# Kernel optimization log

Hardware: AMD Instinct MI355X
Metric: run time of the kernel (lower is better)

Reference implementation:

```python
import jax, jax.numpy as jnp
import numpy as np

DIM = 768
NUM_HEADS = 12
HEAD_DIM = DIM // NUM_HEADS
SCALE = HEAD_DIM ** -0.5
B, N = 16, 640  # N = 8*8 + 24*24


def setup_inputs() -> dict:
    key = jax.random.key(0)
    ks = jax.random.split(key, 4)
    x = jax.random.normal(ks[0], (B, N, DIM), dtype=jnp.float32)
    # weights stored input-major: y = x @ W + b (equiv. to torch Linear with W = weight.T)
    qkv_w = jax.random.normal(ks[1], (DIM, 3 * DIM), dtype=jnp.float32) * (DIM ** -0.5)
    qkv_b = jnp.zeros((3 * DIM,), dtype=jnp.float32)
    proj_w = jax.random.normal(ks[2], (DIM, DIM), dtype=jnp.float32) * (DIM ** -0.5)
    proj_b = jnp.zeros((DIM,), dtype=jnp.float32)
    w = jnp.ones((2,), dtype=jnp.float32)
    return {"x": x, "qkv_w": qkv_w, "qkv_b": qkv_b, "proj_w": proj_w,
            "proj_b": proj_b, "w": w, "t_h": 8, "t_w": 8, "s_h": 24, "s_w": 24}


def reference(x, qkv_w, qkv_b, proj_w, proj_b, w, t_h, t_w, s_h, s_w):
    b, n, c = x.shape
    qkv = (x @ qkv_w + qkv_b).reshape(b, n, 3, NUM_HEADS, HEAD_DIM)
    qkv = jnp.transpose(qkv, (2, 0, 3, 1, 4))  # [3, B, H, N, D]
    q, k, v = qkv[0], qkv[1], qkv[2]
    attn = jnp.einsum('bhnd,bhmd->bhnm', q, k) * SCALE  # [B,H,N,N]
    attn0 = jax.nn.softmax(attn, axis=-1)
    attn1 = jnp.square(jax.nn.relu(attn))
    ws = jax.nn.softmax(w)  # exp(w_i)/sum(exp(w)) blend weights
    attn = attn0 * ws[0] + attn1 * ws[1]
    out = jnp.einsum('bhnm,bhmd->bhnd', attn, v)  # [B,H,N,D]
    out = jnp.transpose(out, (0, 2, 1, 3)).reshape(b, n, c)
    return out @ proj_w + proj_b
```

## Files before the change

kernel.cpp:

```cpp
#include <hip/hip_runtime.h>
#include <hip/hip_bf16.h>

typedef __attribute__((ext_vector_type(8))) short short8;
typedef __attribute__((ext_vector_type(4))) float floatx4;
typedef __hip_bfloat16 bf16;

#define DIM 768
#define NH 12
#define HD 64
#define BB 16
#define NN 640
#define BH (BB*NH)
#define MROWS (BB*NN)
#define QKVN (3*DIM)
#define QSCALE 0.18033688011113205f
#define LN2SQ 0.4804530139182014f

#define CVT_BLK (MROWS*DIM/4/256)
#define TRQ_BLK ((QKVN/32)*(DIM/32))
#define TRP_BLK ((DIM/32)*(DIM/32))

__device__ __forceinline__ floatx4 mfma16(short8 a, short8 b, floatx4 c) {
    return __builtin_amdgcn_mfma_f32_16x16x32_bf16(a, b, c, 0, 0, 0);
}

__device__ __forceinline__ void async_ld16(const bf16* g, bf16* l) {
    __builtin_amdgcn_global_load_lds(
        (const __attribute__((address_space(1))) void*)g,
        (__attribute__((address_space(3))) void*)l, 16, 0, 0);
}

__device__ __forceinline__ unsigned pack_trunc(float a, float b) {
    return __builtin_amdgcn_perm(__float_as_uint(b), __float_as_uint(a), 0x07060302u);
}

__device__ __forceinline__ float fexp2(float x) {
#if __has_builtin(__builtin_amdgcn_exp2f)
    return __builtin_amdgcn_exp2f(x);
#else
    return exp2f(x);
#endif
}

__global__ void prep_all(const float* __restrict__ x,
                         const float* __restrict__ qkv_w,
                         const float* __restrict__ proj_w,
                         bf16* __restrict__ xb,
                         bf16* __restrict__ qwT,
                         bf16* __restrict__ pwT)
{
    __shared__ float tile[32][33];
    const int id = blockIdx.x;
    const int t = threadIdx.x;

    if (id < CVT_BLK) {
        int i = id * 256 + t;
        float4 v = ((const float4*)x)[i];
        bf16* p = xb + (size_t)i * 4;
        p[0] = __float2bfloat16(v.x);
        p[1] = __float2bfloat16(v.y);
        p[2] = __float2bfloat16(v.z);
        p[3] = __float2bfloat16(v.w);
        return;
    }

    const float* src; bf16* dst; int C, bx, by;
    if (id < CVT_BLK + TRQ_BLK) {
        int j = id - CVT_BLK;
        bx = j % (QKVN/32); by = j / (QKVN/32);
        src = qkv_w; dst = qwT; C = QKVN;
    } else {
        int j = id - CVT_BLK - TRQ_BLK;
        bx = j % (DIM/32); by = j / (DIM/32);
        src = proj_w; dst = pwT; C = DIM;
    }
    const int R = DIM;
    const int tx = t & 31, ty = t >> 5;
    for (int j = 0; j < 4; ++j)
        tile[ty + j*8][tx] = src[(size_t)(by*32 + ty + j*8) * C + bx*32 + tx];
    __syncthreads();
    for (int j = 0; j < 4; ++j)
        dst[(size_t)(bx*32 + ty + j*8) * R + by*32 + tx] = __float2bfloat16(tile[tx][ty + j*8]);
}

template<int MODE>
__global__ __launch_bounds__(256) void gemm_bt(
    const bf16* __restrict__ A, const bf16* __restrict__ B, const float* __restrict__ bias,
    int M, int N, int K,
    bf16* __restrict__ outb, bf16* __restrict__ vTo, float* __restrict__ outf)
{
    __shared__ __align__(16) bf16 As[2][128*64];
    __shared__ __align__(16) bf16 Bs[2][128*64];

    const int t = threadIdx.x;
    const int lane = t & 63, wave = t >> 6;
    const int l15 = lane & 15, quad = lane >> 4;
    const int wm = (wave >> 1) * 64, wn = (wave & 1) * 64;
    const int m0 = blockIdx.y * 128, n0 = blockIdx.x * 128;

    floatx4 acc[4][4];
    floatx4 zero = {0.f, 0.f, 0.f, 0.f};
    for (int i = 0; i < 4; ++i)
        for (int j = 0; j < 4; ++j)
            acc[i][j] = zero;

    const int trow = t >> 3;
    const int gc = ((t & 7) ^ (trow & 7)) << 3;
    const bf16* aA = A + (size_t)(m0 + trow) * K + gc;
    const bf16* aB = B + (size_t)(n0 + trow) * K + gc;
    const int lb = wave * 512;

    for (int s = 0; s < 4; ++s) {
        async_ld16(aA + (size_t)s*32*K, &As[0][s*2048 + lb]);
        async_ld16(aB + (size_t)s*32*K, &Bs[0][s*2048 + lb]);
    }

    const int sw = l15 & 7;
    const int nit = K >> 6;
    for (int kt = 0; kt < nit; ++kt) {
        const int cur = kt & 1;
        __syncthreads();
        if (kt + 1 < nit) {
            const bf16* pA = aA + (size_t)(kt+1)*64;
            const bf16* pB = aB + (size_t)(kt+1)*64;
            for (int s = 0; s < 4; ++s) {
                async_ld16(pA + (size_t)s*32*K, &As[cur^1][s*2048 + lb]);
                async_ld16(pB + (size_t)s*32*K, &Bs[cur^1][s*2048 + lb]);
            }
        }
        short8 af0[4], af1[4], bf0[4], bf1[4];
        for (int fm = 0; fm < 4; ++fm) {
            int base = (wm + fm*16 + l15) * 64 + ((quad ^ sw) << 3);
            af0[fm] = *(const short8*)(&As[cur][base]);
            af1[fm] = *(const short8*)(&As[cur][base ^ 32]);
        }
        for (int fn = 0; fn < 4; ++fn) {
            int base = (wn + fn*16 + l15) * 64 + ((quad ^ sw) << 3);
            bf0[fn] = *(const short8*)(&Bs[cur][base]);
            bf1[fn] = *(const short8*)(&Bs[cur][base ^ 32]);
        }
        for (int fm = 0; fm < 4; ++fm)
            for (int fn = 0; fn < 4; ++fn) {
                acc[fm][fn] = mfma16(af0[fm], bf0[fn], acc[fm][fn]);
                acc[fm][fn] = mfma16(af1[fm], bf1[fn], acc[fm][fn]);
            }
    }

    if (MODE == 0 && n0 >= 2*DIM) {
        bf16* T4 = &As[0][0] + wave * 2048;
        const int bh   = (m0 / NN) * NH + ((n0 + wn) >> 6) - 24;
        const int tokb = (m0 % NN) + wm;
        for (int fn = 0; fn < 4; ++fn) {
            int n = n0 + wn + fn*16 + l15;
            float bn = bias[n];
            for (int fm = 0; fm < 4; ++fm) {
                float v0 = acc[fm][fn][0] + bn, v1 = acc[fm][fn][1] + bn;
                float v2 = acc[fm][fn][2] + bn, v3 = acc[fm][fn][3] + bn;
                *(uint2*)(T4 + fm*512 + l15*32 + quad*4) =
                    make_uint2(pack_trunc(v0, v1), pack_trunc(v2, v3));
            }
            uint4 r0 = *(const uint4*)(T4 + quad*512 + l15*32);
            uint4 r1 = *(const uint4*)(T4 + quad*512 + l15*32 + 8);
            int d = fn*16 + l15;
            bf16* dst = vTo + ((size_t)bh * HD + d) * NN + tokb + quad*16;
            *(uint4*)dst = r0;
            *(uint4*)(dst + 8) = r1;
        }
        return;
    }

    for (int fm = 0; fm < 4; ++fm) {
        for (int fn = 0; fn < 4; ++fn) {
            int n = n0 + wn + fn*16 + l15;
            float bn = bias[n];
            for (int r = 0; r < 4; ++r) {
                int m = m0 + wm + fm*16 + quad*4 + r;
                float v = acc[fm][fn][r] + bn;
                if (MODE == 0) {
                    if (n < DIM) v *= QSCALE;
                    outb[(size_t)m * N + n] = __float2bfloat16(v);
                } else {
                    outf[(size_t)m * N + n] = v;
                }
            }
        }
    }
}

__global__ __launch_bounds__(256) void attn_kernel(
    const bf16* __restrict__ qkv, const bf16* __restrict__ vT,
    const float* __restrict__ w2, bf16* __restrict__ ao)
{
    const int bh = blockIdx.x;
    const int b = bh / NH, h = bh - b * NH;
    const int t = threadIdx.x;
    const int wave = t >> 6, lane = t & 63;
    const int l15 = lane & 15, quad = lane >> 4;
    const int qrow0 = blockIdx.y * 64 + wave * 16;

    float w0 = w2[0], w1 = w2[1];
    float wmx = fmaxf(w0, w1);
    float e0 = __expf(w0 - wmx), e1 = __expf(w1 - wmx);
    float ws0 = e0 / (e0 + e1);
    float ws1 = (1.0f - ws0) * LN2SQ;

    __shared__ __align__(16) bf16 Kb[2][64*64];
    __shared__ __align__(16) bf16 Vb[2][64*64];
    __shared__ __align__(16) bf16 Ps[4][16*72];
    __shared__ __align__(16) bf16 Pr[4][16*72];

    const bf16* kb = qkv + (size_t)(b*NN)*QKVN + DIM + h*HD;
    const bf16* vb = vT + (size_t)bh * HD * NN;

    const bf16* qr = qkv + (size_t)(b*NN + qrow0 + l15) * QKVN + h*HD;
    short8 aq0 = *(const short8*)(qr + quad*8);
    short8 aq1 = *(const short8*)(qr + 32 + quad*8);

    const int srow = t >> 3;
    const int gc   = ((lane & 7) ^ (lane >> 3)) << 3;
    const bf16* kst = kb + (size_t)srow * QKVN + gc;
    const bf16* vst = vb + (size_t)srow * NN + gc;
    const int lb0 = (wave * 64) * 8;
    const int lb1 = (256 + wave * 64) * 8;

    async_ld16(kst,                     &Kb[0][lb0]);
    async_ld16(kst + (size_t)32 * QKVN, &Kb[0][lb1]);
    async_ld16(vst,                     &Vb[0][lb0]);
    async_ld16(vst + (size_t)32 * NN,   &Vb[0][lb1]);

    floatx4 zero = {0.f, 0.f, 0.f, 0.f};
    floatx4 accS[4], accR[4];
    for (int i = 0; i < 4; ++i) { accS[i] = zero; accR[i] = zero; }
    float lsum = 0.f;

    const int sw = l15 & 7;
    const int fbase = l15 * 64 + ((quad ^ sw) << 3);

    unsigned* PsW = (unsigned*)&Ps[wave][0];
    unsigned* PrW = (unsigned*)&Pr[wave][0];
    const int wb = l15*36 + quad*2;
    const bf16* PsR = &Ps[wave][l15*72 + quad*8];
    const bf16* PrR = &Pr[wave][l15*72 + quad*8];

#pragma unroll 2
    for (int kt = 0; kt < 10; ++kt) {
        const int cur = kt & 1;
        __syncthreads();
        if (kt + 1 < 10) {
            kst += (size_t)64 * QKVN;
            vst += 64;
            async_ld16(kst,                     &Kb[cur^1][lb0]);
            async_ld16(kst + (size_t)32 * QKVN, &Kb[cur^1][lb1]);
            async_ld16(vst,                     &Vb[cur^1][lb0]);
            async_ld16(vst + (size_t)32 * NN,   &Vb[cur^1][lb1]);
        }

        const bf16* Kc = &Kb[cur][0];
        const bf16* Vc = &Vb[cur][0];

        floatx4 s[4];
        for (int I = 0; I < 4; ++I) {
            short8 aklo = *(const short8*)(Kc + fbase + I*1024);
            short8 akhi = *(const short8*)(Kc + ((fbase + I*1024) ^ 32));
            s[I] = zero;
            s[I] = mfma16(aklo, aq0, s[I]);
            s[I] = mfma16(akhi, aq1, s[I]);
        }

        short8 bvlo[4], bvhi[4];
        for (int dt = 0; dt < 4; ++dt) {
            bvlo[dt] = *(const short8*)(Vc + fbase + dt*1024);
            bvhi[dt] = *(const short8*)(Vc + ((fbase + dt*1024) ^ 32));
        }

        for (int I = 0; I < 4; ++I) {
            float ex[4], rq[4];
            for (int r = 0; r < 4; ++r) {
                ex[r] = fexp2(s[I][r]);
                float m = fmaxf(s[I][r], 0.f);
                rq[r] = m * m;
                lsum += ex[r];
            }
            *(uint2*)(PsW + wb + I*8) = make_uint2(pack_trunc(ex[0],ex[1]), pack_trunc(ex[2],ex[3]));
            *(uint2*)(PrW + wb + I*8) = make_uint2(pack_trunc(rq[0],rq[1]), pack_trunc(rq[2],rq[3]));
        }

        short8 paSlo = *(const short8*)PsR;
        short8 paShi = *(const short8*)(PsR + 32);
        short8 paRlo = *(const short8*)PrR;
        short8 paRhi = *(const short8*)(PrR + 32);

        for (int dt = 0; dt < 4; ++dt) {
            accS[dt] = mfma16(paSlo, bvlo[dt], accS[dt]);
            accS[dt] = mfma16(paShi, bvhi[dt], accS[dt]);
            accR[dt] = mfma16(paRlo, bvlo[dt], accR[dt]);
            accR[dt] = mfma16(paRhi, bvhi[dt], accR[dt]);
        }
    }

    lsum += __shfl_xor(lsum, 16);
    lsum += __shfl_xor(lsum, 32);
    float invq[4];
    for (int r = 0; r < 4; ++r)
        invq[r] = 1.0f / __shfl(lsum, quad*4 + r);

    for (int dt = 0; dt < 4; ++dt) {
        for (int r = 0; r < 4; ++r) {
            float v = ws0 * accS[dt][r] * invq[r] + ws1 * accR[dt][r];
            int tok = qrow0 + quad*4 + r;
            ao[((size_t)(b * NN + tok)) * DIM + h * HD + dt*16 + l15] = __float2bfloat16(v);
        }
    }
}


extern "C" void kernel_launch(void* const* d_in, const int* in_sizes, int n_in,
                              void* d_out, int out_size, void* d_ws, size_t ws_size,
                              hipStream_t stream) {
    const float* x      = (const float*)d_in[0];
    const float* qkv_w  = (const float*)d_in[1];
    const float* qkv_b  = (const float*)d_in[2];
    const float* proj_w = (const float*)d_in[3];
    const float* proj_b = (const float*)d_in[4];
    const float* w2     = (const float*)d_in[5];
    float* out = (float*)d_out;

    bf16* xb   = (bf16*)d_ws;
    bf16* qwT  = xb   + (size_t)MROWS * DIM;
    bf16* pwT  = qwT  + (size_t)QKVN * DIM;
    bf16* qkvb = pwT  + (size_t)DIM * DIM;
    bf16* vT   = qkvb + (size_t)MROWS * QKVN;
    bf16* ao   = xb;

    prep_all<<<CVT_BLK + TRQ_BLK + TRP_BLK, 256, 0, stream>>>(
        x, qkv_w, proj_w, xb, qwT, pwT);

    gemm_bt<0><<<dim3(QKVN / 128, MROWS / 128), 256, 0, stream>>>(
        xb, qwT, qkv_b, MROWS, QKVN, DIM, qkvb, vT, nullptr);

    attn_kernel<<<dim3(BH, NN / 64), 256, 0, stream>>>(qkvb, vT, w2, ao);

    gemm_bt<1><<<dim3(DIM / 128, MROWS / 128), 256, 0, stream>>>(
        ao, pwT, proj_b, MROWS, DIM, DIM, nullptr, nullptr, out);
}
```

Measured before the change: 219.8 us.

## Remap workgroups across XCDs, swap MFMA operands for vectorized epilogue stores

Measured after the change: 217.7 us. No clear change (-1.0%).

```diff
diff --git a/kernel.cpp b/kernel.cpp
--- a/kernel.cpp
+++ b/kernel.cpp
@@ -34,6 +34,12 @@
     return __builtin_amdgcn_perm(__float_as_uint(b), __float_as_uint(a), 0x07060302u);
 }
 
+__device__ __forceinline__ unsigned pack_rne(float a, float b) {
+    unsigned sa = (unsigned)__bfloat16_as_ushort(__float2bfloat16(a));
+    unsigned sb = (unsigned)__bfloat16_as_ushort(__float2bfloat16(b));
+    return sa | (sb << 16);
+}
+
 __device__ __forceinline__ float fexp2(float x) {
 #if __has_builtin(__builtin_amdgcn_exp2f)
     return __builtin_amdgcn_exp2f(x);
@@ -56,11 +62,8 @@
     if (id < CVT_BLK) {
         int i = id * 256 + t;
         float4 v = ((const float4*)x)[i];
-        bf16* p = xb + (size_t)i * 4;
-        p[0] = __float2bfloat16(v.x);
-        p[1] = __float2bfloat16(v.y);
-        p[2] = __float2bfloat16(v.z);
-        p[3] = __float2bfloat16(v.w);
+        *(uint2*)(xb + (size_t)i * 4) =
+            make_uint2(pack_rne(v.x, v.y), pack_rne(v.z, v.w));
         return;
     }
 
@@ -96,7 +99,13 @@
     const int lane = t & 63, wave = t >> 6;
     const int l15 = lane & 15, quad = lane >> 4;
     const int wm = (wave >> 1) * 64, wn = (wave & 1) * 64;
-    const int m0 = blockIdx.y * 128, n0 = blockIdx.x * 128;
+
+    constexpr int GX  = (MODE == 0) ? (QKVN/128) : (DIM/128);
+    constexpr int NWG = GX * (MROWS/128);
+    constexpr int CHUNK = NWG / 8;
+    int lin = blockIdx.y * GX + blockIdx.x;
+    lin = (lin & 7) * CHUNK + (lin >> 3);
+    const int m0 = (lin / GX) * 128, n0 = (lin % GX) * 128;
 
     floatx4 acc[4][4];
     floatx4 zero = {0.f, 0.f, 0.f, 0.f};
@@ -141,28 +150,32 @@
         }
         for (int fm = 0; fm < 4; ++fm)
             for (int fn = 0; fn < 4; ++fn) {
-                acc[fm][fn] = mfma16(af0[fm], bf0[fn], acc[fm][fn]);
-                acc[fm][fn] = mfma16(af1[fm], bf1[fn], acc[fm][fn]);
+                acc[fm][fn] = mfma16(bf0[fn], af0[fm], acc[fm][fn]);
+                acc[fm][fn] = mfma16(bf1[fn], af1[fm], acc[fm][fn]);
             }
     }
 
     if (MODE == 0 && n0 >= 2*DIM) {
-        bf16* T4 = &As[0][0] + wave * 2048;
+        bf16* S = &As[0][0] + wave * 2048;
+        unsigned short* Su = (unsigned short*)S;
         const int bh   = (m0 / NN) * NH + ((n0 + wn) >> 6) - 24;
         const int tokb = (m0 % NN) + wm;
+        const int dl = lane >> 2, cc = (lane & 3) * 16;
         for (int fn = 0; fn < 4; ++fn) {
-            int n = n0 + wn + fn*16 + l15;
-            float bn = bias[n];
+            int nb = n0 + wn + fn*16 + quad*4;
+            float4 bv = *(const float4*)(bias + nb);
+            float bvr[4] = {bv.x, bv.y, bv.z, bv.w};
             for (int fm = 0; fm < 4; ++fm) {
-                float v0 = acc[fm][fn][0] + bn, v1 = acc[fm][fn][1] + bn;
-                float v2 = acc[fm][fn][2] + bn, v3 = acc[fm][fn][3] + bn;
-                *(uint2*)(T4 + fm*512 + l15*32 + quad*4) =
-                    make_uint2(pack_trunc(v0, v1), pack_trunc(v2, v3));
-            }
-            uint4 r0 = *(const uint4*)(T4 + quad*512 + l15*32);
-            uint4 r1 = *(const uint4*)(T4 + quad*512 + l15*32 + 8);
-            int d = fn*16 + l15;
-            bf16* dst = vTo + ((size_t)bh * HD + d) * NN + tokb + quad*16;
+#pragma unroll
+                for (int r = 0; r < 4; ++r) {
+                    float v = acc[fm][fn][r] + bvr[r];
+                    Su[(quad*4 + r)*72 + fm*16 + l15] =
+                        (unsigned short)(__float_as_uint(v) >> 16);
+                }
+            }
+            uint4 r0 = *(const uint4*)(S + dl*72 + cc);
+            uint4 r1 = *(const uint4*)(S + dl*72 + cc + 8);
+            bf16* dst = vTo + ((size_t)bh * HD + fn*16 + dl) * NN + tokb + cc;
             *(uint4*)dst = r0;
             *(uint4*)(dst + 8) = r1;
         }
@@ -170,18 +183,32 @@
     }
 
     for (int fm = 0; fm < 4; ++fm) {
-        for (int fn = 0; fn < 4; ++fn) {
-            int n = n0 + wn + fn*16 + l15;
-            float bn = bias[n];
-            for (int r = 0; r < 4; ++r) {
-                int m = m0 + wm + fm*16 + quad*4 + r;
-                float v = acc[fm][fn][r] + bn;
-                if (MODE == 0) {
-                    if (n < DIM) v *= QSCALE;
-                    outb[(size_t)m * N + n] = __float2bfloat16(v);
-                } else {
-                    outf[(size_t)m * N + n] = v;
+        int m = m0 + wm + fm*16 + l15;
+        if (MODE == 0) {
+            bf16* row = outb + (size_t)m * N;
+            for (int fn = 0; fn < 4; ++fn) {
+                int n = n0 + wn + fn*16 + quad*4;
+                float4 bv = *(const float4*)(bias + n);
+                float v0 = acc[fm][fn][0] + bv.x;
+                float v1 = acc[fm][fn][1] + bv.y;
+                float v2 = acc[fm][fn][2] + bv.z;
+                float v3 = acc[fm][fn][3] + bv.w;
+                if (n < DIM) {
+                    v0 *= QSCALE; v1 *= QSCALE; v2 *= QSCALE; v3 *= QSCALE;
                 }
+                *(uint2*)(row + n) = make_uint2(pack_rne(v0, v1), pack_rne(v2, v3));
+            }
+        } else {
+            float* row = outf + (size_t)m * N;
+            for (int fn = 0; fn < 4; ++fn) {
+                int n = n0 + wn + fn*16 + quad*4;
+                float4 bv = *(const float4*)(bias + n);
+                float4 v;
+                v.x = acc[fm][fn][0] + bv.x;
+                v.y = acc[fm][fn][1] + bv.y;
+                v.z = acc[fm][fn][2] + bv.z;
+                v.w = acc[fm][fn][3] + bv.w;
+                *(float4*)(row + n) = v;
             }
         }
     }
@@ -191,12 +218,15 @@
     const bf16* __restrict__ qkv, const bf16* __restrict__ vT,
     const float* __restrict__ w2, bf16* __restrict__ ao)
 {
-    const int bh = blockIdx.x;
+    int lin = blockIdx.y * BH + blockIdx.x;
+    int j = lin >> 3;
+    const int bh = (lin & 7) + 8 * (j / 10);
+    const int qt = j % 10;
     const int b = bh / NH, h = bh - b * NH;
     const int t = threadIdx.x;
     const int wave = t >> 6, lane = t & 63;
     const int l15 = lane & 15, quad = lane >> 4;
-    const int qrow0 = blockIdx.y * 64 + wave * 16;
+    const int qrow0 = qt * 64 + wave * 16;
 
     float w0 = w2[0], w1 = w2[1];
     float wmx = fmaxf(w0, w1);
```
